# Performance work log

Measured on AMD Instinct MI355X. Metric: run time of the kernel, lower is better.

Reference implementation:

```python
import math
import jax, jax.numpy as jnp
import numpy as np
from jax import lax

D = 384; NHEAD = 12; NLAYERS = 4; H = 128; WIN = (128, 24); NS = (1, 10); B = 256; CONV_C = 128

def _interleave(s, c):
    # [s0,c0,s1,c1,...] along last dim (matches 0::2=sin, 1::2=cos)
    return jnp.stack([s, c], axis=-1).reshape(s.shape[:-1] + (s.shape[-1] * 2,))

def _pos_encoding():
    d3 = D // 3
    div = jnp.exp(jnp.arange(0, d3, 2, dtype=jnp.float32) * (-math.log(10000.0) / d3))
    coord = jnp.arange(H, dtype=jnp.float32) - H // 2
    pe1d = _interleave(jnp.sin(coord[:, None] * div), jnp.cos(coord[:, None] * div))  # (H, d3)
    pe_y = jnp.broadcast_to(pe1d[:, None, :], (H, H, d3))
    pe_x = jnp.broadcast_to(pe1d[None, :, :], (H, H, d3))
    ws = jnp.array(WIN, dtype=jnp.float32)
    pe_w = _interleave(jnp.sin(ws[:, None] * div), jnp.cos(ws[:, None] * div))  # (2, d3)
    pe_yx = jnp.concatenate([pe_y, pe_x], axis=-1)  # (H, H, 2*d3)
    pe = jnp.concatenate([
        jnp.broadcast_to(pe_yx[:, :, None, :], (H, H, len(WIN), 2 * d3)),
        jnp.broadcast_to(pe_w[None, None, :, :], (H, H, len(WIN), d3))], axis=-1)
    return pe  # (H, H, 2, D)

def _windows(img3, pos, ws):
    # img3: (B,3,H,W); pos: (n,2) int. Crop [y1:y2, x1:x2] then zero-pad bottom/right to ws x ws.
    hw = ws // 2
    y = jnp.clip(pos[:, 0], 0, H - 1); x = jnp.clip(pos[:, 1], 0, H - 1)
    y1 = jnp.maximum(0, y - hw); y2 = jnp.minimum(H, y + hw)
    x1 = jnp.maximum(0, x - hw); x2 = jnp.minimum(H, x + hw)
    r = jnp.arange(ws)
    rows = y1[:, None] + r; cols = x1[:, None] + r  # (n, ws)
    mask = (rows < y2[:, None])[:, :, None] & (cols < x2[:, None])[:, None, :]  # (n, ws, ws)
    win = img3[:, :, jnp.clip(rows, 0, H - 1)[:, :, None], jnp.clip(cols, 0, H - 1)[:, None, :]]  # (B,3,n,ws,ws)
    win = jnp.where(mask[None, None], win, 0.0)
    return jnp.transpose(win, (0, 2, 1, 3, 4))  # (B, n, 3, ws, ws)

def _layer_norm(x, g, b):
    m = x.mean(-1, keepdims=True)
    v = ((x - m) ** 2).mean(-1, keepdims=True)
    return (x - m) / jnp.sqrt(v + 1e-5) * g + b

def _encoder_layer(x, Wqkv, bqkv, Wo, bo, g1, b1, g2, b2, W1, bf1, W2, bf2):
    Bsz, S, _ = x.shape
    dh = D // NHEAD
    qkv = x @ Wqkv.T + bqkv
    q, k, v = jnp.split(qkv, 3, axis=-1)
    heads = lambda t: t.reshape(Bsz, S, NHEAD, dh).transpose(0, 2, 1, 3)
    q, k, v = heads(q), heads(k), heads(v)
    att = jax.nn.softmax(jnp.einsum('bhqd,bhkd->bhqk', q, k) / math.sqrt(dh), axis=-1)
    o = jnp.einsum('bhqk,bhkd->bhqd', att, v).transpose(0, 2, 1, 3).reshape(Bsz, S, D)
    x = _layer_norm(x + o @ Wo.T + bo, g1, b1)
    ff = jax.nn.relu(x @ W1.T + bf1) @ W2.T + bf2
    return _layer_norm(x + ff, g2, b2)

def _normalize(v):
    return v / jnp.maximum(jnp.linalg.norm(v, axis=1, keepdims=True), 1e-12)

def _forward(pos0, pos1, rgb_image, conv_w, conv_b, ext_w, ext_b, proj_w, proj_b,
             Wqkv, bqkv, Wo, bo, ln1g, ln1b, ln2g, ln2b, Wff1, bff1, Wff2, bff2,
             rw1, rb1, rw2, rb2, uw1, ub1, uw2, ub2):
    Bsz = rgb_image.shape[0]
    img3 = rgb_image[:, :3]
    win0 = _windows(img3, pos0, WIN[0]).reshape(Bsz * NS[0], 3, WIN[0], WIN[0])
    win1 = _windows(img3, pos1, WIN[1])  # (B, 10, 3, 24, 24)
    h = lax.conv_general_dilated(win0, conv_w, (4, 4), 'SAME')
    h = jax.nn.relu(h + conv_b[None, :, None, None])
    f0 = (h.mean((2, 3)) @ ext_w.T + ext_b).reshape(Bsz, NS[0], D)
    f1 = win1.reshape(Bsz, NS[1], -1) @ proj_w.T + proj_b  # (B,10,D)
    feats = jnp.concatenate([f0, f1], axis=1)  # (B, 11, D)
    pe = _pos_encoding()
    pp = jnp.concatenate([
        jnp.concatenate([pos0, jnp.zeros((NS[0], 1), pos0.dtype)], axis=1),
        jnp.concatenate([pos1, jnp.ones((NS[1], 1), pos1.dtype)], axis=1)], axis=0)  # (11, 3)
    pf = pe[pp[:, 0], pp[:, 1], pp[:, 2]]  # (11, D)
    x = feats + pf[None]
    for i in range(NLAYERS):
        x = _encoder_layer(x, Wqkv[i], bqkv[i], Wo[i], bo[i], ln1g[i], ln1b[i],
                           ln2g[i], ln2b[i], Wff1[i], bff1[i], Wff2[i], bff2[i])
    m = x.mean(axis=1)
    r = jax.nn.relu(m @ rw1.T + rb1) @ rw2.T + rb2
    r1, r2 = r[:, :3], r[:, 3:]
    r2 = r2 - jnp.sum(r1 * r2, axis=1, keepdims=True) * r1
    r3 = jnp.cross(r1, r2)
    R = jnp.concatenate([_normalize(r1), _normalize(r2), _normalize(r3)], axis=1)
    uv = jax.nn.sigmoid(jax.nn.relu(m @ uw1.T + ub1) @ uw2.T + ub2)
    return (uv, R)

def setup_inputs():
    key = jax.random.key(0)
    ks = iter(jax.random.split(key, 40))
    w = lambda *s: jax.random.normal(next(ks), s, jnp.float32) * 0.02
    return dict(
        rgb_image=jax.random.uniform(next(ks), (B, 4, H, H), jnp.float32),
        pos0=jax.random.randint(next(ks), (NS[0], 2), 0, H).astype(jnp.int32),
        pos1=jax.random.randint(next(ks), (NS[1], 2), 0, H).astype(jnp.int32),
        conv_w=w(CONV_C, 3, 7, 7), conv_b=jnp.zeros((CONV_C,), jnp.float32),
        ext_w=w(D, CONV_C), ext_b=jnp.zeros((D,), jnp.float32),
        proj_w=w(D, WIN[1] * WIN[1] * 3), proj_b=jnp.zeros((D,), jnp.float32),
        Wqkv=w(NLAYERS, 3 * D, D), bqkv=jnp.zeros((NLAYERS, 3 * D), jnp.float32),
        Wo=w(NLAYERS, D, D), bo=jnp.zeros((NLAYERS, D), jnp.float32),
        ln1g=jnp.ones((NLAYERS, D), jnp.float32), ln1b=jnp.zeros((NLAYERS, D), jnp.float32),
        ln2g=jnp.ones((NLAYERS, D), jnp.float32), ln2b=jnp.zeros((NLAYERS, D), jnp.float32),
        Wff1=w(NLAYERS, 2048, D), bff1=jnp.zeros((NLAYERS, 2048), jnp.float32),
        Wff2=w(NLAYERS, D, 2048), bff2=jnp.zeros((NLAYERS, D), jnp.float32),
        rw1=w(D, D), rb1=jnp.zeros((D,), jnp.float32),
        rw2=w(6, D), rb2=jnp.zeros((6,), jnp.float32),
        uw1=w(D, D), ub1=jnp.zeros((D,), jnp.float32),
        uw2=w(2, D), ub2=jnp.zeros((2,), jnp.float32),
    )

def reference(rgb_image, pos0, pos1, conv_w, conv_b, ext_w, ext_b, proj_w, proj_b,
              Wqkv, bqkv, Wo, bo, ln1g, ln1b, ln2g, ln2b, Wff1, bff1, Wff2, bff2,
              rw1, rb1, rw2, rb2, uw1, ub1, uw2, ub2):
    return _forward(pos0, pos1, rgb_image, conv_w, conv_b, ext_w, ext_b, proj_w, proj_b,
                    Wqkv, bqkv, Wo, bo, ln1g, ln1b, ln2g, ln2b, Wff1, bff1, Wff2, bff2,
                    rw1, rb1, rw2, rb2, uw1, ub1, uw2, ub2)
```

## Files before the change

### kernel.cpp

```cpp
#include <hip/hip_runtime.h>
#include <hip/hip_bf16.h>

#define B_ 256
#define S_ 11
#define D_ 384
#define NHEAD_ 12

typedef const float* bfp;
typedef __attribute__((ext_vector_type(8))) __bf16 bf16x8;
typedef __attribute__((ext_vector_type(4))) float f32x4;

__device__ __forceinline__ bf16x8 ld8_b64(const __bf16* p) {
    union { unsigned long long q[2]; bf16x8 v; } u;
    u.q[0] = *reinterpret_cast<const unsigned long long*>(p);
    u.q[1] = *reinterpret_cast<const unsigned long long*>(p + 4);
    return u.v;
}

__device__ __forceinline__ void gl16(const __bf16* g, __bf16* l) {
    __builtin_amdgcn_global_load_lds(
        (const __attribute__((address_space(1))) void*)g,
        (__attribute__((address_space(3))) void*)l, 16, 0, 0);
}

__global__ void prep_k(const float* __restrict__ proj_w, const float* __restrict__ Wqkv,
                       const float* __restrict__ Wo, const float* __restrict__ Wff1,
                       const float* __restrict__ Wff2,
                       __bf16* __restrict__ projWb, __bf16* __restrict__ WqkvB,
                       __bf16* __restrict__ WoB, __bf16* __restrict__ Wff1B,
                       __bf16* __restrict__ Wff2B,
                       const float* __restrict__ cw, __bf16* __restrict__ wpad,
                       const int* __restrict__ pos0, const int* __restrict__ pos1,
                       float* __restrict__ pf)
{
    int i = blockIdx.x * 256 + threadIdx.x;
    const float* s; __bf16* d; int off;
    if      (i < 165888)  { s = proj_w; d = projWb; off = i; }
    else if (i < 608256)  { s = Wqkv;   d = WqkvB;  off = i - 165888; }
    else if (i < 755712)  { s = Wo;     d = WoB;    off = i - 608256; }
    else if (i < 1542144) { s = Wff1;   d = Wff1B;  off = i - 755712; }
    else if (i < 2328576) { s = Wff2;   d = Wff2B;  off = i - 1542144; }
    else if (i < 2331648) {
        int e = i - 2328576;
        int r = e >> 5, g = e & 31;
        if (g >= 24) return;
        union { __bf16 h[8]; uint4 u; } w;
        #pragma unroll
        for (int kx = 0; kx < 8; ++kx) {
            float v = 0.f;
            if (g < 21 && kx < 7) v = cw[(size_t)r * 147 + g * 7 + kx];
            w.h[kx] = (__bf16)v;
        }
        *reinterpret_cast<uint4*>(&wpad[(size_t)r * 192 + g * 8]) = w.u;
        return;
    }
    else if (i < 2332032) {
        int dd0 = i - 2331648;
        const float c1 = -logf(10000.f) / 128.f;
        for (int ss = 0; ss < 11; ++ss) {
            int py, px, pw;
            if (ss == 0) { py = pos0[0]; px = pos0[1]; pw = 0; }
            else { py = pos1[(ss - 1) * 2]; px = pos1[(ss - 1) * 2 + 1]; pw = 1; }
            float coordv; int dd = dd0;
            if (dd0 < 128) coordv = (float)(py - 64);
            else if (dd0 < 256) { coordv = (float)(px - 64); dd = dd0 - 128; }
            else { coordv = (pw == 0) ? 128.f : 24.f; dd = dd0 - 256; }
            int ii = dd >> 1;
            float div = expf((float)(2 * ii) * c1);
            float ang = coordv * div;
            pf[ss * 384 + dd0] = (dd & 1) ? cosf(ang) : sinf(ang);
        }
        return;
    }
    else return;
    float4 v = reinterpret_cast<const float4*>(s)[off];
    union { __bf16 h[4]; unsigned long long u; } p;
    p.h[0] = (__bf16)v.x; p.h[1] = (__bf16)v.y;
    p.h[2] = (__bf16)v.z; p.h[3] = (__bf16)v.w;
    reinterpret_cast<unsigned long long*>(d)[off] = p.u;
}

__global__ __launch_bounds__(256) void gemm_bb_k(
    const __bf16* __restrict__ A, const __bf16* __restrict__ W,
    const float* __restrict__ bias, const float* __restrict__ resid,
    void* __restrict__ C_, int M, int N, int K, int mode, int outBf16, int kChunk)
{
    __shared__ __align__(16) __bf16 AsF[2][8192];
    __shared__ __align__(16) __bf16 WsF[2][4096];
    const int tid = threadIdx.x;
    const int bm = blockIdx.y * 128, bn = blockIdx.x * 64;
    const int z = blockIdx.z;
    int kStart = 0, kEnd = K;
    if (kChunk) { kStart = z * kChunk; kEnd = min(K, kStart + kChunk); }
    const int lane = tid & 63, wv = tid >> 6;
    const int wrA = (wv >> 1) * 64, wcW = (wv & 1) * 32;
    const int lr = lane & 15, lk = lane >> 4;
    size_t gaoff[4], gwoff[2];
    #pragma unroll
    for (int k = 0; k < 4; ++k) {
        int c = tid + k * 256; int r = c >> 3; int j = (c & 7) ^ (r & 7);
        gaoff[k] = (size_t)(bm + r) * K + j * 8;
    }
    #pragma unroll
    for (int k = 0; k < 2; ++k) {
        int c = tid + k * 256; int r = c >> 3; int j = (c & 7) ^ (r & 7);
        gwoff[k] = (size_t)(bn + r) * K + j * 8;
    }
    f32x4 acc[4][2] = {};

#define STAGE_(bf, kk) do {                                       \
        gl16(A + gaoff[0] + (kk), &AsF[bf][(wv << 9)]);           \
        gl16(A + gaoff[1] + (kk), &AsF[bf][2048 + (wv << 9)]);    \
        gl16(A + gaoff[2] + (kk), &AsF[bf][4096 + (wv << 9)]);    \
        gl16(A + gaoff[3] + (kk), &AsF[bf][6144 + (wv << 9)]);    \
        gl16(W + gwoff[0] + (kk), &WsF[bf][(wv << 9)]);           \
        gl16(W + gwoff[1] + (kk), &WsF[bf][2048 + (wv << 9)]);    \
    } while (0)

    STAGE_(0, kStart);
    __syncthreads();
    int cur = 0;
    for (int k0 = kStart; k0 < kEnd; k0 += 64) {
        if (k0 + 64 < kEnd) STAGE_(cur ^ 1, k0 + 64);
        const __bf16* Ab = AsF[cur];
        const __bf16* Wb = WsF[cur];
        #pragma unroll
        for (int s = 0; s < 2; ++s) {
            int j = s * 4 + lk;
            int rw0 = wcW + lr, rw1_ = wcW + 16 + lr;
            bf16x8 w0 = *reinterpret_cast<const bf16x8*>(&Wb[rw0 * 64 + ((j ^ (rw0 & 7)) << 3)]);
            bf16x8 w1 = *reinterpret_cast<const bf16x8*>(&Wb[rw1_ * 64 + ((j ^ (rw1_ & 7)) << 3)]);
            #pragma unroll
            for (int m = 0; m < 4; ++m) {
                int ra = wrA + m * 16 + lr;
                bf16x8 a = *reinterpret_cast<const bf16x8*>(&Ab[ra * 64 + ((j ^ (ra & 7)) << 3)]);
                acc[m][0] = __builtin_amdgcn_mfma_f32_16x16x32_bf16(a, w0, acc[m][0], 0, 0, 0);
                acc[m][1] = __builtin_amdgcn_mfma_f32_16x16x32_bf16(a, w1, acc[m][1], 0, 0, 0);
            }
        }
        __syncthreads();
        cur ^= 1;
    }
#undef STAGE_
    if (kChunk) {
        float* Cp = (float*)C_ + (size_t)z * M * N;
        #pragma unroll
        for (int m = 0; m < 4; ++m)
            #pragma unroll
            for (int n = 0; n < 2; ++n) {
                int col = bn + wcW + n * 16 + lr;
                #pragma unroll
                for (int i = 0; i < 4; ++i) {
                    int row = bm + wrA + m * 16 + lk * 4 + i;
                    Cp[(size_t)row * N + col] = acc[m][n][i];
                }
            }
    } else {
        #pragma unroll
        for (int m = 0; m < 4; ++m)
            #pragma unroll
            for (int n = 0; n < 2; ++n) {
                int col = bn + wcW + n * 16 + lr;
                float bcol = bias[col];
                #pragma unroll
                for (int i = 0; i < 4; ++i) {
                    int row = bm + wrA + m * 16 + lk * 4 + i;
                    float v = acc[m][n][i] + bcol;
                    if (mode == 1) v = fmaxf(v, 0.f);
                    if (mode == 2) v += resid[(size_t)row * N + col];
                    if (outBf16) ((__bf16*)C_)[(size_t)row * N + col] = (__bf16)v;
                    else         ((float*)C_)[(size_t)row * N + col] = v;
                }
            }
    }
}

__global__ __launch_bounds__(256) void convgemm_k(
    bfp __restrict__ img, const __bf16* __restrict__ wpad, bfp __restrict__ cb,
    const int* __restrict__ pos0, float* __restrict__ f0pre)
{
    __shared__ __align__(16) __bf16 Wlds[64][200];
    __shared__ __align__(16) __bf16 P[3][12][136];
    const int tid = threadIdx.x;
    const int blk = blockIdx.x;
    const int b = blk >> 3;
    const int bn = ((blk >> 2) & 1) * 64;
    const int mtg = blk & 3;
    int y = min(max(pos0[0], 0), 127), x = min(max(pos0[1], 0), 127);
    int y1 = max(0, y - 64), y2 = min(128, y + 64);
    int x1 = max(0, x - 64), x2 = min(128, x + 64);
    const int lane = tid & 63, wv = tid >> 6;
    const int wr = (wv >> 1) * 32, wc = (wv & 1) * 32;
    const int lr = lane & 15, lk = lane >> 4;
    const int oyl = wr >> 5;
    const int ox0 = lr, ox1 = 16 + lr;

    for (int e = tid; e < 1536; e += 256) {
        int r = e / 24, g = e - r * 24;
        uint4 q = *reinterpret_cast<const uint4*>(&wpad[(size_t)(bn + r) * 192 + g * 8]);
        *reinterpret_cast<uint4*>(&Wlds[r][g * 8]) = q;
    }

    float s0 = 0.f, s1 = 0.f;
    const float bc0 = cb[bn + wc + lr];
    const float bc1 = cb[bn + wc + 16 + lr];

    for (int t = 0; t < 4; ++t) {
        int mt = mtg * 4 + t;
        __syncthreads();
        for (int e = tid; e < 2448; e += 256) {
            int c = e / 816, rem = e - c * 816;
            int r2 = rem / 68, ip2 = (rem - r2 * 68) * 2;
            int rl = mt * 8 - 1 + r2;
            bool rok = (rl >= 0) && ((y1 + rl) < y2);
            const float* row = img + ((size_t)(b * 4 + c) * 128 + y1 + rl) * 128 + x1;
            int cl0 = ip2 - 1, cl1 = ip2;
            float v0 = 0.f, v1 = 0.f;
            if (rok && cl0 >= 0 && (x1 + cl0) < x2) v0 = row[cl0];
            if (rok && (x1 + cl1) < x2)             v1 = row[cl1];
            union { __bf16 h[2]; unsigned int u; } p;
            p.h[0] = (__bf16)v0; p.h[1] = (__bf16)v1;
            *reinterpret_cast<unsigned int*>(&P[c][r2][ip2]) = p.u;
        }
        __syncthreads();
        f32x4 acc[2][2] = {};
        #pragma unroll
        for (int kk = 0; kk < 6; ++kk) {
            int g = kk * 4 + lk;
            int c = g / 7, ky = g - c * 7;
            if (g >= 21) { c = 0; ky = 0; }
            const __bf16* prow = &P[c][oyl * 4 + ky][0];
            bf16x8 a0 = ld8_b64(prow + ox0 * 4);
            bf16x8 a1 = ld8_b64(prow + ox1 * 4);
            bf16x8 w0 = *reinterpret_cast<const bf16x8*>(&Wlds[wc + lr][g * 8]);
            bf16x8 w1 = *reinterpret_cast<const bf16x8*>(&Wlds[wc + 16 + lr][g * 8]);
            acc[0][0] = __builtin_amdgcn_mfma_f32_16x16x32_bf16(a0, w0, acc[0][0], 0, 0, 0);
            acc[0][1] = __builtin_amdgcn_mfma_f32_16x16x32_bf16(a0, w1, acc[0][1], 0, 0, 0);
            acc[1][0] = __builtin_amdgcn_mfma_f32_16x16x32_bf16(a1, w0, acc[1][0], 0, 0, 0);
            acc[1][1] = __builtin_amdgcn_mfma_f32_16x16x32_bf16(a1, w1, acc[1][1], 0, 0, 0);
        }
        #pragma unroll
        for (int m = 0; m < 2; ++m)
            #pragma unroll
            for (int i = 0; i < 4; ++i) {
                s0 += fmaxf(acc[m][0][i] + bc0, 0.f);
                s1 += fmaxf(acc[m][1][i] + bc1, 0.f);
            }
    }
    s0 += __shfl_xor(s0, 16); s0 += __shfl_xor(s0, 32);
    s1 += __shfl_xor(s1, 16); s1 += __shfl_xor(s1, 32);
    if (lk == 0) {
        atomicAdd(&f0pre[b * 128 + bn + wc + lr],      s0 * (1.f / 1024.f));
        atomicAdd(&f0pre[b * 128 + bn + wc + 16 + lr], s1 * (1.f / 1024.f));
    }
}

__global__ void win1_k(bfp __restrict__ img, const int* __restrict__ pos1,
                       __bf16* __restrict__ w1)
{
    int i = blockIdx.x * 256 + threadIdx.x;
    if (i >= B_ * 10 * 1728) return;
    int cc = i % 24, r = (i / 24) % 24, c = (i / 576) % 3, s = (i / 1728) % 10, b = i / 17280;
    int y = min(max(pos1[s * 2], 0), 127), x = min(max(pos1[s * 2 + 1], 0), 127);
    int y1 = max(0, y - 12), y2 = min(128, y + 12);
    int x1 = max(0, x - 12), x2 = min(128, x + 12);
    float v = 0.f;
    if ((y1 + r) < y2 && (x1 + cc) < x2)
        v = img[((size_t)(b * 4 + c) * 128 + (y1 + r)) * 128 + (x1 + cc)];
    w1[i] = (__bf16)v;
}

__global__ void assemble_k(const float* __restrict__ f0pre, bfp __restrict__ ew,
                           bfp __restrict__ eb,
                           const float* __restrict__ p0, const float* __restrict__ p1,
                           const float* __restrict__ projb,
                           const float* __restrict__ pf, float* __restrict__ x,
                           __bf16* __restrict__ xb)
{
    int i = blockIdx.x * 256 + threadIdx.x;
    if (i >= B_ * S_ * D_) return;
    int d = i % 384, s = (i / 384) % 11, b = i / (384 * 11);
    float f;
    if (s == 0) {
        float acc = eb[d];
        const float* pre = f0pre + b * 128;
        const float* wrow = ew + (size_t)d * 128;
        #pragma unroll 4
        for (int co = 0; co < 128; ++co) acc += pre[co] * wrow[co];
        f = acc;
    } else {
        size_t o = ((size_t)(b * 10) + (s - 1)) * 384 + d;
        f = p0[o] + p1[o] + projb[d];
    }
    float v = f + pf[s * 384 + d];
    x[i] = v;
    xb[i] = (__bf16)v;
}

__global__ __launch_bounds__(128) void attn_k(const float* __restrict__ qkv,
                                              __bf16* __restrict__ obuf)
{
    int b = blockIdx.x / NHEAD_, h = blockIdx.x % NHEAD_;
    __shared__ float q[11][32], k[11][32], v[11][32], att[11][12];
    for (int e = threadIdx.x; e < 352; e += 128) {
        int s = e >> 5, d = e & 31;
        size_t base = (size_t)(b * 11 + s) * 1152 + h * 32 + d;
        q[s][d] = qkv[base];
        k[s][d] = qkv[base + 384];
        v[s][d] = qkv[base + 768];
    }
    __syncthreads();
    if (threadIdx.x < 121) {
        int i = threadIdx.x / 11, j = threadIdx.x % 11;
        float s = 0.f;
        #pragma unroll
        for (int d = 0; d < 32; ++d) s += q[i][d] * k[j][d];
        att[i][j] = s * 0.17677669529663687f;
    }
    __syncthreads();
    if (threadIdx.x < 11) {
        int i = threadIdx.x;
        float mx = att[i][0];
        for (int j = 1; j < 11; ++j) mx = fmaxf(mx, att[i][j]);
        float e_[11], sum = 0.f;
        for (int j = 0; j < 11; ++j) { e_[j] = expf(att[i][j] - mx); sum += e_[j]; }
        float inv = 1.f / sum;
        for (int j = 0; j < 11; ++j) att[i][j] = e_[j] * inv;
    }
    __syncthreads();
    for (int e = threadIdx.x; e < 352; e += 128) {
        int i = e >> 5, d = e & 31;
        float s = 0.f;
        #pragma unroll
        for (int j = 0; j < 11; ++j) s += att[i][j] * v[j][d];
        obuf[(size_t)(b * 11 + i) * 384 + h * 32 + d] = (__bf16)s;
    }
}

__global__ __launch_bounds__(512) void ln_k(const float* __restrict__ parts, int nparts,
                                            const float* __restrict__ resid,
                                            const float* __restrict__ bias,
                                            bfp g, bfp be, float* __restrict__ xo,
                                            __bf16* __restrict__ xb)
{
    int row = blockIdx.x * 8 + (threadIdx.x >> 6);
    int lane = threadIdx.x & 63;
    const size_t MN = (size_t)2816 * 384;
    float v[6];
    float s = 0.f, sq = 0.f;
    #pragma unroll
    for (int j = 0; j < 6; ++j) {
        int d = lane + 64 * j;
        size_t off = (size_t)row * 384 + d;
        float t = resid[off] + bias[d];
        for (int z = 0; z < nparts; ++z) t += parts[z * MN + off];
        v[j] = t; s += t; sq += t * t;
    }
    #pragma unroll
    for (int o = 32; o >= 1; o >>= 1) { s += __shfl_xor(s, o); sq += __shfl_xor(sq, o); }
    float mean = s * (1.f / 384.f);
    float var = sq * (1.f / 384.f) - mean * mean;
    float inv = rsqrtf(var + 1e-5f);
    float* xr = xo + (size_t)row * 384;
    __bf16* xbr = xb + (size_t)row * 384;
    #pragma unroll
    for (int j = 0; j < 6; ++j) {
        int d = lane + 64 * j;
        float o = (v[j] - mean) * inv * g[d] + be[d];
        xr[d] = o;
        xbr[d] = (__bf16)o;
    }
}

__global__ __launch_bounds__(384) void headfused_k(
    const float* __restrict__ X,
    bfp __restrict__ rw1, bfp __restrict__ rb1, bfp __restrict__ uw1, bfp __restrict__ ub1,
    bfp __restrict__ rw2, bfp __restrict__ rb2, bfp __restrict__ uw2, bfp __restrict__ ub2,
    float* __restrict__ out)
{
    __shared__ float m[384], h1s[384], h2s[384];
    int b = blockIdx.x, d = threadIdx.x;
    float s = 0.f;
    for (int si = 0; si < 11; ++si) s += X[((size_t)b * 11 + si) * 384 + d];
    m[d] = s * (1.f / 11.f);
    __syncthreads();
    float a1 = rb1[d], a2 = ub1[d];
    const float4* r4 = reinterpret_cast<const float4*>(rw1 + (size_t)d * 384);
    const float4* u4 = reinterpret_cast<const float4*>(uw1 + (size_t)d * 384);
    for (int k4 = 0; k4 < 96; ++k4) {
        float4 wv1 = r4[k4], wv2 = u4[k4];
        const float* mk = &m[k4 * 4];
        a1 += mk[0] * wv1.x + mk[1] * wv1.y + mk[2] * wv1.z + mk[3] * wv1.w;
        a2 += mk[0] * wv2.x + mk[1] * wv2.y + mk[2] * wv2.z + mk[3] * wv2.w;
    }
    h1s[d] = fmaxf(a1, 0.f);
    h2s[d] = fmaxf(a2, 0.f);
    __syncthreads();
    if (d < 64) {
        int lane = d;
        float acc[8] = {};
        for (int dd = lane; dd < 384; dd += 64) {
            float v1 = h1s[dd], v2 = h2s[dd];
            #pragma unroll
            for (int o = 0; o < 6; ++o) acc[o] += v1 * rw2[o * 384 + dd];
            acc[6] += v2 * uw2[dd];
            acc[7] += v2 * uw2[384 + dd];
        }
        #pragma unroll
        for (int o = 0; o < 8; ++o)
            #pragma unroll
            for (int off = 32; off >= 1; off >>= 1) acc[o] += __shfl_xor(acc[o], off);
        if (lane == 0) {
            float r[6];
            for (int o = 0; o < 6; ++o) r[o] = acc[o] + rb2[o];
            float u0 = acc[6] + ub2[0], u1 = acc[7] + ub2[1];
            float dot12 = r[0] * r[3] + r[1] * r[4] + r[2] * r[5];
            float q2x = r[3] - dot12 * r[0], q2y = r[4] - dot12 * r[1], q2z = r[5] - dot12 * r[2];
            float q3x = r[1] * q2z - r[2] * q2y;
            float q3y = r[2] * q2x - r[0] * q2z;
            float q3z = r[0] * q2y - r[1] * q2x;
            float n1 = fmaxf(sqrtf(r[0]*r[0] + r[1]*r[1] + r[2]*r[2]), 1e-12f);
            float n2 = fmaxf(sqrtf(q2x*q2x + q2y*q2y + q2z*q2z), 1e-12f);
            float n3 = fmaxf(sqrtf(q3x*q3x + q3y*q3y + q3z*q3z), 1e-12f);
            out[b * 2 + 0] = 1.f / (1.f + expf(-u0));
            out[b * 2 + 1] = 1.f / (1.f + expf(-u1));
            float* R = out + B_ * 2 + b * 9;
            R[0] = r[0] / n1; R[1] = r[1] / n1; R[2] = r[2] / n1;
            R[3] = q2x / n2;  R[4] = q2y / n2;  R[5] = q2z / n2;
            R[6] = q3x / n3;  R[7] = q3y / n3;  R[8] = q3z / n3;
        }
    }
}

extern "C" void kernel_launch(void* const* d_in, const int* in_sizes, int n_in,
                              void* d_out, int out_size, void* d_ws, size_t ws_size,
                              hipStream_t stream)
{
    bfp rgb     = (bfp)d_in[0];
    const int* pos0 = (const int*)d_in[1];
    const int* pos1 = (const int*)d_in[2];
    bfp conv_w  = (bfp)d_in[3];
    bfp conv_b  = (bfp)d_in[4];
    bfp ext_w   = (bfp)d_in[5];
    bfp ext_b   = (bfp)d_in[6];
    bfp proj_w  = (bfp)d_in[7];
    bfp proj_b  = (bfp)d_in[8];
    bfp Wqkv    = (bfp)d_in[9];
    bfp bqkv    = (bfp)d_in[10];
    bfp Wo      = (bfp)d_in[11];
    bfp bo      = (bfp)d_in[12];
    bfp ln1g    = (bfp)d_in[13];
    bfp ln1b    = (bfp)d_in[14];
    bfp ln2g    = (bfp)d_in[15];
    bfp ln2b    = (bfp)d_in[16];
    bfp Wff1    = (bfp)d_in[17];
    bfp bff1    = (bfp)d_in[18];
    bfp Wff2    = (bfp)d_in[19];
    bfp bff2    = (bfp)d_in[20];
    bfp rw1     = (bfp)d_in[21];
    bfp rb1     = (bfp)d_in[22];
    bfp rw2     = (bfp)d_in[23];
    bfp rb2     = (bfp)d_in[24];
    bfp uw1     = (bfp)d_in[25];
    bfp ub1     = (bfp)d_in[26];
    bfp uw2     = (bfp)d_in[27];
    bfp ub2     = (bfp)d_in[28];

    float* ws = (float*)d_ws;
    float*  X      = ws;
    float*  QKV    = ws + 2162688;
    float*  F0PRE  = QKV + 1081344;
    float*  PP0    = QKV + 1114112;
    float*  PP1    = QKV + 1114112 + 983040;
    __bf16* OBUFb  = (__bf16*)(ws + 5406720);
    __bf16* FFH16  = (__bf16*)(ws + 6144000);
    __bf16* WIN1F16= FFH16;
    float*  PF     = ws + 9027584;
    __bf16* Xb     = (__bf16*)(ws + 9130112);
    __bf16* projWb = (__bf16*)(ws + 9670784);
    __bf16* WqkvB  = (__bf16*)(ws + 10002560);
    __bf16* WoB    = (__bf16*)(ws + 10887296);
    __bf16* Wff1B  = (__bf16*)(ws + 11182208);
    __bf16* Wff2B  = (__bf16*)(ws + 12755072);
    __bf16* WpadC  = (__bf16*)(ws + 14327936);

    hipMemsetAsync(F0PRE, 0, 256 * 128 * sizeof(float), stream);

    prep_k<<<9110, 256, 0, stream>>>(proj_w, Wqkv, Wo, Wff1, Wff2,
                                     projWb, WqkvB, WoB, Wff1B, Wff2B,
                                     conv_w, WpadC, pos0, pos1, PF);

    convgemm_k<<<2048, 256, 0, stream>>>(rgb, WpadC, conv_b, pos0, F0PRE);
    win1_k<<<(B_ * 10 * 1728 + 255) / 256, 256, 0, stream>>>(rgb, pos1, WIN1F16);
    gemm_bb_k<<<dim3(6, 20, 2), 256, 0, stream>>>(WIN1F16, projWb, nullptr, nullptr,
                                                  PP0, 2560, 384, 1728, 0, 0, 896);
    assemble_k<<<(B_ * S_ * D_ + 255) / 256, 256, 0, stream>>>(
        F0PRE, ext_w, ext_b, PP0, PP1, proj_b, PF, X, Xb);

    for (int i = 0; i < 4; ++i) {
        gemm_bb_k<<<dim3(18, 22), 256, 0, stream>>>(
            Xb, WqkvB + (size_t)i * 1152 * 384, bqkv + i * 1152, nullptr, QKV,
            2816, 1152, 384, 0, 0, 0);
        attn_k<<<B_ * NHEAD_, 128, 0, stream>>>(QKV, OBUFb);
        gemm_bb_k<<<dim3(6, 22, 2), 256, 0, stream>>>(
            OBUFb, WoB + (size_t)i * 384 * 384, nullptr, nullptr, QKV,
            2816, 384, 384, 0, 0, 192);
        ln_k<<<352, 512, 0, stream>>>(QKV, 2, X, bo + i * 384,
                                      ln1g + i * 384, ln1b + i * 384, X, Xb);
        gemm_bb_k<<<dim3(32, 22), 256, 0, stream>>>(
            Xb, Wff1B + (size_t)i * 2048 * 384, bff1 + i * 2048, nullptr, FFH16,
            2816, 2048, 384, 1, 1, 0);
        gemm_bb_k<<<dim3(6, 22, 3), 256, 0, stream>>>(
            FFH16, Wff2B + (size_t)i * 384 * 2048, nullptr, nullptr, QKV,
            2816, 384, 2048, 0, 0, 704);
        ln_k<<<352, 512, 0, stream>>>(QKV, 3, X, bff2 + i * 384,
                                      ln2g + i * 384, ln2b + i * 384, X, Xb);
    }

    headfused_k<<<256, 384, 0, stream>>>(X, rw1, rb1, uw1, ub1,
                                         rw2, rb2, uw2, ub2, (float*)d_out);
}
```

Before: 488.9 us.

## Pre-pad image to bf16 and double-buffer conv tile loads; emit QKV in bf16

A new kernel writes a zero-padded bf16 copy of the cropped image. The conv GEMM then stages its tiles with async global-to-LDS loads into a double buffer, so the next tile loads while the current one computes, instead of doing per-element fp32 loads and conversions between barriers. Separately, the QKV GEMM now writes bf16 and attention reads bf16, which halves that traffic at some cost in precision. This adds an extra kernel launch and a pass over the image, and the workspace layout is moved around to make room.

```diff
diff --git a/kernel.cpp b/kernel.cpp
--- a/kernel.cpp
+++ b/kernel.cpp
@@ -80,6 +80,32 @@
     reinterpret_cast<unsigned long long*>(d)[off] = p.u;
 }
 
+__global__ void pimg_k(bfp __restrict__ img, const int* __restrict__ pos0,
+                       __bf16* __restrict__ pimg)
+{
+    int i = blockIdx.x * 256 + threadIdx.x;
+    if (i >= 1824768) return;
+    int col8 = i % 18, t = i / 18;
+    int row = t % 132; t /= 132;
+    int ch = t % 3; int b = t / 3;
+    int y = min(max(pos0[0], 0), 127), x = min(max(pos0[1], 0), 127);
+    int y1 = max(0, y - 64), y2 = min(128, y + 64);
+    int x1 = max(0, x - 64), x2 = min(128, x + 64);
+    int iy = y1 + row - 1;
+    bool rok = (row >= 1) && (iy < y2);
+    const float* src = img + ((size_t)(b * 4 + ch) * 128 + iy) * 128;
+    union { __bf16 h[8]; uint4 u; } p;
+    #pragma unroll
+    for (int k = 0; k < 8; ++k) {
+        int cc = col8 * 8 + k;
+        int ix = x1 + cc - 1;
+        float v = 0.f;
+        if (rok && cc >= 1 && ix < x2) v = src[ix];
+        p.h[k] = (__bf16)v;
+    }
+    *reinterpret_cast<uint4*>(&pimg[((size_t)(b * 3 + ch) * 132 + row) * 144 + col8 * 8]) = p.u;
+}
+
 __global__ __launch_bounds__(256) void gemm_bb_k(
     const __bf16* __restrict__ A, const __bf16* __restrict__ W,
     const float* __restrict__ bias, const float* __restrict__ resid,
@@ -176,60 +202,59 @@
 }
 
 __global__ __launch_bounds__(256) void convgemm_k(
-    bfp __restrict__ img, const __bf16* __restrict__ wpad, bfp __restrict__ cb,
-    const int* __restrict__ pos0, float* __restrict__ f0pre)
+    const __bf16* __restrict__ pimg, const __bf16* __restrict__ wpad,
+    bfp __restrict__ cb, float* __restrict__ f0pre)
 {
     __shared__ __align__(16) __bf16 Wlds[64][200];
-    __shared__ __align__(16) __bf16 P[3][12][136];
+    __shared__ __align__(16) __bf16 P[2][4896];
     const int tid = threadIdx.x;
     const int blk = blockIdx.x;
     const int b = blk >> 3;
     const int bn = ((blk >> 2) & 1) * 64;
     const int mtg = blk & 3;
-    int y = min(max(pos0[0], 0), 127), x = min(max(pos0[1], 0), 127);
-    int y1 = max(0, y - 64), y2 = min(128, y + 64);
-    int x1 = max(0, x - 64), x2 = min(128, x + 64);
     const int lane = tid & 63, wv = tid >> 6;
     const int wr = (wv >> 1) * 32, wc = (wv & 1) * 32;
     const int lr = lane & 15, lk = lane >> 4;
     const int oyl = wr >> 5;
     const int ox0 = lr, ox1 = 16 + lr;
 
+    size_t poff[3]; bool pval[3];
+    #pragma unroll
+    for (int p = 0; p < 3; ++p) {
+        int c = tid + p * 256;
+        pval[p] = (c < 612);
+        int col8 = c % 17, rowi = c / 17;
+        int r2 = rowi % 12, c3 = rowi / 12;
+        poff[p] = ((size_t)(b * 3 + c3) * 132 + r2) * 144 + col8 * 8;
+    }
+#define STAGEP_(buf, mt) do {                                                 \
+        if (pval[0]) gl16(pimg + poff[0] + (size_t)(mt) * 1152, &P[buf][(0 + (wv << 6)) * 8]);      \
+        if (pval[1]) gl16(pimg + poff[1] + (size_t)(mt) * 1152, &P[buf][(256 + (wv << 6)) * 8]);    \
+        if (pval[2]) gl16(pimg + poff[2] + (size_t)(mt) * 1152, &P[buf][(512 + (wv << 6)) * 8]);    \
+    } while (0)
+
+    STAGEP_(0, mtg * 4);
     for (int e = tid; e < 1536; e += 256) {
         int r = e / 24, g = e - r * 24;
         uint4 q = *reinterpret_cast<const uint4*>(&wpad[(size_t)(bn + r) * 192 + g * 8]);
         *reinterpret_cast<uint4*>(&Wlds[r][g * 8]) = q;
     }
+    __syncthreads();
 
     float s0 = 0.f, s1 = 0.f;
     const float bc0 = cb[bn + wc + lr];
     const float bc1 = cb[bn + wc + 16 + lr];
 
     for (int t = 0; t < 4; ++t) {
-        int mt = mtg * 4 + t;
-        __syncthreads();
-        for (int e = tid; e < 2448; e += 256) {
-            int c = e / 816, rem = e - c * 816;
-            int r2 = rem / 68, ip2 = (rem - r2 * 68) * 2;
-            int rl = mt * 8 - 1 + r2;
-            bool rok = (rl >= 0) && ((y1 + rl) < y2);
-            const float* row = img + ((size_t)(b * 4 + c) * 128 + y1 + rl) * 128 + x1;
-            int cl0 = ip2 - 1, cl1 = ip2;
-            float v0 = 0.f, v1 = 0.f;
-            if (rok && cl0 >= 0 && (x1 + cl0) < x2) v0 = row[cl0];
-            if (rok && (x1 + cl1) < x2)             v1 = row[cl1];
-            union { __bf16 h[2]; unsigned int u; } p;
-            p.h[0] = (__bf16)v0; p.h[1] = (__bf16)v1;
-            *reinterpret_cast<unsigned int*>(&P[c][r2][ip2]) = p.u;
-        }
-        __syncthreads();
+        if (t < 3) STAGEP_((t + 1) & 1, mtg * 4 + t + 1);
+        const __bf16* Pb = P[t & 1];
         f32x4 acc[2][2] = {};
         #pragma unroll
         for (int kk = 0; kk < 6; ++kk) {
             int g = kk * 4 + lk;
             int c = g / 7, ky = g - c * 7;
             if (g >= 21) { c = 0; ky = 0; }
-            const __bf16* prow = &P[c][oyl * 4 + ky][0];
+            const __bf16* prow = &Pb[(c * 12 + oyl * 4 + ky) * 136];
             bf16x8 a0 = ld8_b64(prow + ox0 * 4);
             bf16x8 a1 = ld8_b64(prow + ox1 * 4);
             bf16x8 w0 = *reinterpret_cast<const bf16x8*>(&Wlds[wc + lr][g * 8]);
@@ -246,7 +271,9 @@
                 s0 += fmaxf(acc[m][0][i] + bc0, 0.f);
                 s1 += fmaxf(acc[m][1][i] + bc1, 0.f);
             }
-    }
+        __syncthreads();
+    }
+#undef STAGEP_
     s0 += __shfl_xor(s0, 16); s0 += __shfl_xor(s0, 32);
     s1 += __shfl_xor(s1, 16); s1 += __shfl_xor(s1, 32);
     if (lk == 0) {
@@ -297,7 +324,7 @@
     xb[i] = (__bf16)v;
 }
 
-__global__ __launch_bounds__(128) void attn_k(const float* __restrict__ qkv,
+__global__ __launch_bounds__(128) void attn_k(const __bf16* __restrict__ qkv,
                                               __bf16* __restrict__ obuf)
 {
     int b = blockIdx.x / NHEAD_, h = blockIdx.x % NHEAD_;
@@ -305,9 +332,9 @@
     for (int e = threadIdx.x; e < 352; e += 128) {
         int s = e >> 5, d = e & 31;
         size_t base = (size_t)(b * 11 + s) * 1152 + h * 32 + d;
-        q[s][d] = qkv[base];
-        k[s][d] = qkv[base + 384];
-        v[s][d] = qkv[base + 768];
+        q[s][d] = (float)qkv[base];
+        k[s][d] = (float)qkv[base + 384];
+        v[s][d] = (float)qkv[base + 768];
     }
     __syncthreads();
     if (threadIdx.x < 121) {
@@ -468,14 +495,16 @@
 
     float* ws = (float*)d_ws;
     float*  X      = ws;
+    __bf16* PIMG   = (__bf16*)(ws + 1081344);
     float*  QKV    = ws + 2162688;
-    float*  F0PRE  = QKV + 1081344;
-    float*  PP0    = QKV + 1114112;
-    float*  PP1    = QKV + 1114112 + 983040;
+    __bf16* QKVb   = (__bf16*)QKV;
+    float*  PP0    = ws + 3276800;
+    float*  PP1    = ws + 4259840;
     __bf16* OBUFb  = (__bf16*)(ws + 5406720);
     __bf16* FFH16  = (__bf16*)(ws + 6144000);
     __bf16* WIN1F16= FFH16;
     float*  PF     = ws + 9027584;
+    float*  F0PRE  = ws + 9031808;
     __bf16* Xb     = (__bf16*)(ws + 9130112);
     __bf16* projWb = (__bf16*)(ws + 9670784);
     __bf16* WqkvB  = (__bf16*)(ws + 10002560);
@@ -489,8 +518,8 @@
     prep_k<<<9110, 256, 0, stream>>>(proj_w, Wqkv, Wo, Wff1, Wff2,
                                      projWb, WqkvB, WoB, Wff1B, Wff2B,
                                      conv_w, WpadC, pos0, pos1, PF);
-
-    convgemm_k<<<2048, 256, 0, stream>>>(rgb, WpadC, conv_b, pos0, F0PRE);
+    pimg_k<<<7128, 256, 0, stream>>>(rgb, pos0, PIMG);
+    convgemm_k<<<2048, 256, 0, stream>>>(PIMG, WpadC, conv_b, F0PRE);
     win1_k<<<(B_ * 10 * 1728 + 255) / 256, 256, 0, stream>>>(rgb, pos1, WIN1F16);
     gemm_bb_k<<<dim3(6, 20, 2), 256, 0, stream>>>(WIN1F16, projWb, nullptr, nullptr,
                                                   PP0, 2560, 384, 1728, 0, 0, 896);
@@ -499,9 +528,9 @@
 
     for (int i = 0; i < 4; ++i) {
         gemm_bb_k<<<dim3(18, 22), 256, 0, stream>>>(
-            Xb, WqkvB + (size_t)i * 1152 * 384, bqkv + i * 1152, nullptr, QKV,
-            2816, 1152, 384, 0, 0, 0);
-        attn_k<<<B_ * NHEAD_, 128, 0, stream>>>(QKV, OBUFb);
+            Xb, WqkvB + (size_t)i * 1152 * 384, bqkv + i * 1152, nullptr, QKVb,
+            2816, 1152, 384, 0, 1, 0);
+        attn_k<<<B_ * NHEAD_, 128, 0, stream>>>(QKVb, OBUFb);
         gemm_bb_k<<<dim3(6, 22, 2), 256, 0, stream>>>(
             OBUFb, WoB + (size_t)i * 384 * 384, nullptr, nullptr, QKV,
             2816, 384, 384, 0, 0, 192);
```

After: 457.4 us. 1.07x faster.
